# Kernel optimization log

Measured on AMD Instinct MI355X. Metric: run time of the kernel, lower is better.

Reference implementation:

```python
import jax, jax.numpy as jnp
import numpy as np

N = 50000      # nodes
E = 800000     # edges (before self-loops)
F_IN = 256
H = 4          # heads
C1 = 128
C2 = 64
NCLS = 50
NEG_SLOPE = 0.2


def setup_inputs() -> dict:
    key = jax.random.key(0)
    ks = jax.random.split(key, 12)
    x = jax.random.normal(ks[0], (N, F_IN), dtype=jnp.float32)
    edge_index = jax.random.randint(ks[1], (2, E), 0, N, dtype=jnp.int32)
    s1 = 1.0 / np.sqrt(F_IN)
    s2 = 1.0 / np.sqrt(H * C1)
    s3 = 1.0 / np.sqrt(H * C2)
    return {
        "x": x,
        "edge_index": edge_index,
        "W1": jax.random.normal(ks[2], (F_IN, H * C1), dtype=jnp.float32) * s1,
        "a_src1": jax.random.normal(ks[3], (H, C1), dtype=jnp.float32) * s2,
        "a_dst1": jax.random.normal(ks[4], (H, C1), dtype=jnp.float32) * s2,
        "b1": jnp.zeros((H * C1,), dtype=jnp.float32),
        "W2": jax.random.normal(ks[5], (H * C1, H * C2), dtype=jnp.float32) * s2,
        "a_src2": jax.random.normal(ks[6], (H, C2), dtype=jnp.float32) * s3,
        "a_dst2": jax.random.normal(ks[7], (H, C2), dtype=jnp.float32) * s3,
        "b2": jnp.zeros((H * C2,), dtype=jnp.float32),
        "Wf": jax.random.normal(ks[8], (H * C2, NCLS), dtype=jnp.float32) * s3,
        "bf": jnp.zeros((NCLS,), dtype=jnp.float32),
    }


def _gat_conv(x, src, dst, W, a_src, a_dst, b, heads, ch):
    # h: [N, H, C] transformed features
    h = (x @ W).reshape(N, heads, ch)
    # per-node attention halves (standard GAT decomposition, avoids per-edge d-dim gather for scores)
    asrc = jnp.sum(h * a_src[None], axis=-1)  # [N, H]
    adst = jnp.sum(h * a_dst[None], axis=-1)  # [N, H]
    e = jax.nn.leaky_relu(asrc[src] + adst[dst], NEG_SLOPE)  # [E, H]
    # softmax over edges sharing the same destination node
    m = jax.ops.segment_max(e, dst, num_segments=N)          # [N, H]
    ex = jnp.exp(e - m[dst])
    denom = jax.ops.segment_sum(ex, dst, num_segments=N)     # [N, H]
    alpha = ex / (denom[dst] + 1e-16)                        # [E, H]
    msg = h[src] * alpha[:, :, None]                         # [E, H, C]
    out = jax.ops.segment_sum(msg, dst, num_segments=N)      # [N, H, C]
    return out.reshape(N, heads * ch) + b


def reference(x, edge_index, W1, a_src1, a_dst1, b1, W2, a_src2, a_dst2, b2, Wf, bf):
    # PyG GATConv adds self-loops by default
    loops = jnp.arange(N, dtype=edge_index.dtype)
    src = jnp.concatenate([edge_index[0], loops])
    dst = jnp.concatenate([edge_index[1], loops])
    h = _gat_conv(x, src, dst, W1, a_src1, a_dst1, b1, H, C1)
    h = jax.nn.elu(h)
    # F.dropout is identity in eval mode
    h = _gat_conv(h, src, dst, W2, a_src2, a_dst2, b2, H, C2)
    h = jax.nn.elu(h)
    return h @ Wf + bf
```

## Files before the change

kernel.cpp:

```cpp
#include <hip/hip_runtime.h>
#include <hip/hip_fp16.h>
#include <cmath>

#define NN 50000
#define EE 800000
#define ET 850000
#define HH 4
#define CC1 128
#define CC2 64
#define FIN 256
#define NCLS 50

typedef _Float16 half8_t __attribute__((ext_vector_type(8)));
typedef __attribute__((ext_vector_type(4))) float floatx4;

typedef const __attribute__((address_space(1))) unsigned int* glds_gp_t;
typedef __attribute__((address_space(3))) unsigned int* glds_lp_t;
__device__ __forceinline__ void glds16(const void* g, void* l) {
    __builtin_amdgcn_global_load_lds((glds_gp_t)g, (glds_lp_t)l, 16, 0, 0);
}

#define NB_CAST 12500
#define NB_W1   512
#define NB_W2   512
#define NB_WF   64
#define NB_HIST 3321
__global__ __launch_bounds__(256) void prep_hist(
    const float* __restrict__ x, __half* __restrict__ xb,
    const float* __restrict__ W1, __half* __restrict__ W1t,
    const float* __restrict__ W2, __half* __restrict__ W2t,
    const float* __restrict__ Wf, __half* __restrict__ Wft,
    const int* __restrict__ ei, int* __restrict__ deg)
{
    int b = blockIdx.x;
    if (b < NB_CAST) {
        int t = b * 256 + threadIdx.x;
        float4 v = *(const float4*)(x + 4 * (size_t)t);
        __half2 p[2];
        p[0] = __floats2half2_rn(v.x, v.y);
        p[1] = __floats2half2_rn(v.z, v.w);
        *(uint2*)(xb + 4 * (size_t)t) = *(uint2*)p;
    } else if (b < NB_CAST + NB_W1) {
        int t = (b - NB_CAST) * 256 + threadIdx.x;
        int n = t >> 8, k = t & 255;
        W1t[t] = __float2half(W1[(size_t)k * 512 + n]);
    } else if (b < NB_CAST + NB_W1 + NB_W2) {
        int t = (b - NB_CAST - NB_W1) * 256 + threadIdx.x;
        int n = t >> 9, k = t & 511;
        W2t[t] = __float2half(W2[(size_t)k * 256 + n]);
    } else if (b < NB_CAST + NB_W1 + NB_W2 + NB_WF) {
        int t = (b - NB_CAST - NB_W1 - NB_W2) * 256 + threadIdx.x;
        int n = t >> 8, k = t & 255;
        Wft[t] = (n < NCLS) ? __float2half(Wf[(size_t)k * NCLS + n]) : __float2half(0.f);
    } else {
        int t = (b - NB_CAST - NB_W1 - NB_W2 - NB_WF) * 256 + threadIdx.x;
        if (t < ET) {
            int dst = (t < EE) ? ei[EE + t] : (t - EE);
            atomicAdd(&deg[dst], 1);
        }
    }
}

__global__ __launch_bounds__(256) void gemm_f16_v2(
    const __half* __restrict__ A,
    const __half* __restrict__ Bt,
    __half* __restrict__ C,
    int M, int N, int K)
{
    __shared__ __half As[128 * 32];
    __shared__ __half Bs[128 * 32];
    int tid = threadIdx.x, wave = tid >> 6, lane = tid & 63;
    int wm = (wave >> 1) * 64, wn = (wave & 1) * 64;
    int row0 = blockIdx.x * 128, col0 = blockIdx.y * 128;
    int lm = lane & 15, lq = lane >> 4, kq = lq * 8;
    floatx4 acc[4][4] = {};

    int srow = wave * 32 + (lane >> 2);
    int skk  = (lane & 3) * 8;
    int gra0 = row0 + srow;      if (gra0 >= M) gra0 = M - 1;
    int gra1 = row0 + srow + 16; if (gra1 >= M) gra1 = M - 1;
    const __half* ga0 = A + (size_t)gra0 * K + skk;
    const __half* ga1 = A + (size_t)gra1 * K + skk;
    const __half* gb0 = Bt + (size_t)(col0 + srow) * K + skk;
    const __half* gb1 = Bt + (size_t)(col0 + srow + 16) * K + skk;
    __half* la0 = &As[(wave * 32) * 32];
    __half* la1 = &As[(wave * 32 + 16) * 32];
    __half* lb0 = &Bs[(wave * 32) * 32];
    __half* lb1 = &Bs[(wave * 32 + 16) * 32];

    for (int k0 = 0; k0 < K; k0 += 32) {
        __syncthreads();
        glds16(ga0 + k0, la0);
        glds16(ga1 + k0, la1);
        glds16(gb0 + k0, lb0);
        glds16(gb1 + k0, lb1);
        __syncthreads();

        half8_t af[4], bfr[4];
        #pragma unroll
        for (int mt = 0; mt < 4; ++mt)
            af[mt] = *(const half8_t*)&As[(wm + mt * 16 + lm) * 32 + kq];
        #pragma unroll
        for (int nt = 0; nt < 4; ++nt)
            bfr[nt] = *(const half8_t*)&Bs[(wn + nt * 16 + lm) * 32 + kq];
        #pragma unroll
        for (int mt = 0; mt < 4; ++mt)
            #pragma unroll
            for (int nt = 0; nt < 4; ++nt)
                acc[mt][nt] = __builtin_amdgcn_mfma_f32_16x16x32_f16(
                    af[mt], bfr[nt], acc[mt][nt], 0, 0, 0);
    }

    #pragma unroll
    for (int mt = 0; mt < 4; ++mt) {
        int rbase = row0 + wm + mt * 16 + lq * 4;
        #pragma unroll
        for (int nt = 0; nt < 4; ++nt) {
            int c = col0 + wn + nt * 16 + lm;
            #pragma unroll
            for (int r = 0; r < 4; ++r) {
                int gr = rbase + r;
                if (gr < M) C[(size_t)gr * N + c] = __float2half(acc[mt][nt][r]);
            }
        }
    }
}

__global__ __launch_bounds__(128) void gemm_final(
    const __half* __restrict__ A,
    const __half* __restrict__ Bt,
    const float* __restrict__ bias,
    float* __restrict__ out, int M)
{
    __shared__ __half As[128 * 40];
    __shared__ __half Bs[64 * 40];
    int tid = threadIdx.x, wave = tid >> 6, lane = tid & 63;
    int row0 = blockIdx.x * 128;
    int lm = lane & 15, lq = lane >> 4, kq = lq * 8;
    floatx4 acc[4][4] = {};

    for (int k0 = 0; k0 < 256; k0 += 32) {
        int gr = row0 + tid; if (gr >= M) gr = M - 1;
        const __half* ap = A + (size_t)gr * 256 + k0;
        half8_t a0 = *(const half8_t*)ap;
        half8_t a1 = *(const half8_t*)(ap + 8);
        half8_t a2 = *(const half8_t*)(ap + 16);
        half8_t a3 = *(const half8_t*)(ap + 24);
        const __half* bp = Bt + (size_t)(tid >> 1) * 256 + k0 + (tid & 1) * 16;
        half8_t b0 = *(const half8_t*)bp;
        half8_t b1 = *(const half8_t*)(bp + 8);
        __syncthreads();
        *(half8_t*)&As[tid * 40 + 0]  = a0;
        *(half8_t*)&As[tid * 40 + 8]  = a1;
        *(half8_t*)&As[tid * 40 + 16] = a2;
        *(half8_t*)&As[tid * 40 + 24] = a3;
        *(half8_t*)&Bs[(tid >> 1) * 40 + (tid & 1) * 16]     = b0;
        *(half8_t*)&Bs[(tid >> 1) * 40 + (tid & 1) * 16 + 8] = b1;
        __syncthreads();

        half8_t af[4], bfr[4];
        #pragma unroll
        for (int mt = 0; mt < 4; ++mt)
            af[mt] = *(const half8_t*)&As[(wave * 64 + mt * 16 + lm) * 40 + kq];
        #pragma unroll
        for (int nt = 0; nt < 4; ++nt)
            bfr[nt] = *(const half8_t*)&Bs[(nt * 16 + lm) * 40 + kq];
        #pragma unroll
        for (int mt = 0; mt < 4; ++mt)
            #pragma unroll
            for (int nt = 0; nt < 4; ++nt)
                acc[mt][nt] = __builtin_amdgcn_mfma_f32_16x16x32_f16(
                    af[mt], bfr[nt], acc[mt][nt], 0, 0, 0);
    }

    #pragma unroll
    for (int mt = 0; mt < 4; ++mt) {
        int rbase = row0 + wave * 64 + mt * 16 + lq * 4;
        #pragma unroll
        for (int nt = 0; nt < 4; ++nt) {
            int c = nt * 16 + lm;
            if (c >= NCLS) continue;
            float bv = bias[c];
            #pragma unroll
            for (int r = 0; r < 4; ++r) {
                int gr = rbase + r;
                if (gr < M) out[(size_t)gr * NCLS + c] = acc[mt][nt][r] + bv;
            }
        }
    }
}

template<int C>
__global__ __launch_bounds__(256) void attn_scores3(
    const __half* __restrict__ h, const float* __restrict__ a_src,
    const float* __restrict__ a_dst, float* __restrict__ asrc,
    float* __restrict__ adst, int nwaves)
{
    constexpr int HC = HH * C;
    constexpr int CPL = HC / 64;
    int wave = threadIdx.x >> 6;
    int lane = threadIdx.x & 63;
    int wid0 = blockIdx.x * 4 + wave;
    int c0 = lane * CPL;
    int head = c0 / C;

    for (int n = wid0; n < NN; n += nwaves) {
        const __half* hp = h + (size_t)n * HC + c0;
        float hv[CPL];
        if (CPL == 8) {
            union { uint4 u; __half2 h2[4]; } U;
            U.u = *(const uint4*)hp;
            #pragma unroll
            for (int k = 0; k < 4; ++k) {
                float2 f = __half22float2(U.h2[k]);
                hv[2 * k] = f.x; hv[2 * k + 1] = f.y;
            }
        } else {
            union { uint2 u; __half2 h2[2]; } U;
            U.u = *(const uint2*)hp;
            #pragma unroll
            for (int k = 0; k < 2; ++k) {
                float2 f = __half22float2(U.h2[k]);
                hv[2 * k] = f.x; hv[2 * k + 1] = f.y;
            }
        }
        float s1 = 0.f, s2 = 0.f;
        #pragma unroll
        for (int c = 0; c < CPL; ++c) {
            s1 += hv[c] * a_src[c0 + c];
            s2 += hv[c] * a_dst[c0 + c];
        }
        #pragma unroll
        for (int o = 8; o > 0; o >>= 1) {
            s1 += __shfl_xor(s1, o, 64);
            s2 += __shfl_xor(s2, o, 64);
        }
        if ((lane & 15) == 0) {
            asrc[n * HH + head] = s1;
            adst[n * HH + head] = s2;
        }
    }
}

#define SCAN_NB 25
__global__ __launch_bounds__(256) void scan_fused(
    const int* __restrict__ deg, int* __restrict__ off, int* __restrict__ pos)
{
    __shared__ int ws[4];
    __shared__ int base_s;
    int tid = threadIdx.x;
    int lane = tid & 63, wid = tid >> 6;

    int lim = blockIdx.x * 2048;
    int s0 = 0;
    for (int i = tid; i < lim; i += 256) s0 += deg[i];
    #pragma unroll
    for (int o = 32; o > 0; o >>= 1) s0 += __shfl_xor(s0, o, 64);
    if (lane == 0) ws[wid] = s0;
    __syncthreads();
    if (tid == 0) base_s = ws[0] + ws[1] + ws[2] + ws[3];
    __syncthreads();
    int base = base_s;
    __syncthreads();

    int i0 = blockIdx.x * 2048 + tid * 8;
    int v[8]; int s = 0;
    #pragma unroll
    for (int k = 0; k < 8; ++k) {
        int i = i0 + k;
        v[k] = (i < NN) ? deg[i] : 0;
        s += v[k];
    }
    int sc = s;
    #pragma unroll
    for (int o = 1; o < 64; o <<= 1) {
        int t = __shfl_up(sc, o, 64);
        if (lane >= o) sc += t;
    }
    if (lane == 63) ws[wid] = sc;
    __syncthreads();
    int woff = base;
    for (int w = 0; w < wid; ++w) woff += ws[w];
    int excl = woff + sc - s;
    #pragma unroll
    for (int k = 0; k < 8; ++k) {
        int i = i0 + k;
        if (i < NN) { off[i] = excl; pos[i] = excl; }
        excl += v[k];
    }
    if (blockIdx.x == 0 && tid == 0) off[NN] = ET;
}

__global__ void edge_scatter(const int* __restrict__ ei,
                             int* __restrict__ pos, int* __restrict__ csr_src)
{
    int t = blockIdx.x * blockDim.x + threadIdx.x;
    if (t >= ET) return;
    int src, dst;
    if (t < EE) { src = ei[t]; dst = ei[EE + t]; }
    else        { src = t - EE; dst = t - EE; }
    int p = atomicAdd(&pos[dst], 1);
    csr_src[p] = src;
}

template<int C>
__global__ __launch_bounds__(256) void aggregate8(
    const __half* __restrict__ h, const int* __restrict__ off,
    const int* __restrict__ csr_src, const float* __restrict__ asrc,
    const float* __restrict__ adst, const float* __restrict__ bias,
    __half* __restrict__ outb, int nwaves)
{
    constexpr int HC = HH * C;
    constexpr int LPE = HC / 8;
    constexpr int EPW = 64 / LPE;
    constexpr int UNR = 8;
    __shared__ unsigned int exlds_all[4][64 * HH];
    int wave = threadIdx.x >> 6;
    int lane = threadIdx.x & 63;
    int wid0 = blockIdx.x * 4 + wave;
    unsigned int* exlds = exlds_all[wave];
    int el  = (EPW == 1) ? 0 : (lane >> 5);
    int lel = (EPW == 1) ? lane : (lane & 31);
    int coff = lel * 8;
    int hl = coff / C;

    for (int n = wid0; n < NN; n += nwaves) {
        int start = off[n], end = off[n + 1];
        float4 advv = *(const float4*)(adst + (size_t)n * HH);
        float dh0 = 0.f, dh1 = 0.f, dh2 = 0.f, dh3 = 0.f;
        __half2 acc2[4] = {};

        for (int cb = start; cb < end; cb += 64) {
            int eidx = cb + lane;
            bool valid = eidx < end;
            int s_lane = csr_src[valid ? eidx : end - 1];
            float4 t = *(const float4*)(asrc + (size_t)s_lane * HH);
            float e0 = t.x + advv.x; e0 = e0 > 0.f ? e0 : 0.2f * e0;
            float e1 = t.y + advv.y; e1 = e1 > 0.f ? e1 : 0.2f * e1;
            float e2 = t.z + advv.z; e2 = e2 > 0.f ? e2 : 0.2f * e2;
            float e3 = t.w + advv.w; e3 = e3 > 0.f ? e3 : 0.2f * e3;
            float x0 = valid ? __expf(e0) : 0.f;
            float x1 = valid ? __expf(e1) : 0.f;
            float x2 = valid ? __expf(e2) : 0.f;
            float x3 = valid ? __expf(e3) : 0.f;
            dh0 += x0; dh1 += x1; dh2 += x2; dh3 += x3;
            __half2 xp[4];
            xp[0] = __float2half2_rn(x0);
            xp[1] = __float2half2_rn(x1);
            xp[2] = __float2half2_rn(x2);
            xp[3] = __float2half2_rn(x3);
            *(uint4*)&exlds[lane * 4] = *(uint4*)xp;

            int cnt = end - cb; if (cnt > 64) cnt = 64;
            int jmax = (cnt + UNR * EPW - 1) & ~(UNR * EPW - 1);
            for (int jj = 0; jj < jmax; jj += UNR * EPW) {
                int sidx[UNR]; __half2 xs[UNR];
                union { uint4 u; __half2 h2[4]; } uv[UNR];
                #pragma unroll
                for (int u = 0; u < UNR; ++u) {
                    int e_lo = jj + u * EPW;
                    if (EPW == 1) {
                        sidx[u] = __builtin_amdgcn_readlane(s_lane, e_lo);
                    } else {
                        int sa = __builtin_amdgcn_readlane(s_lane, e_lo);
                        int sb = __builtin_amdgcn_readlane(s_lane, e_lo + 1);
                        sidx[u] = el ? sb : sa;
                    }
                    uv[u].u = *(const uint4*)(h + (size_t)sidx[u] * HC + coff);
                    xs[u] = *(__half2*)&exlds[(e_lo + el) * 4 + hl];
                }
                #pragma unroll
                for (int u = 0; u < UNR; ++u)
                    #pragma unroll
                    for (int k = 0; k < 4; ++k)
                        acc2[k] = __hfma2(xs[u], uv[u].h2[k], acc2[k]);
            }
        }

        #pragma unroll
        for (int o = 32; o > 0; o >>= 1) {
            dh0 += __shfl_xor(dh0, o, 64);
            dh1 += __shfl_xor(dh1, o, 64);
            dh2 += __shfl_xor(dh2, o, 64);
            dh3 += __shfl_xor(dh3, o, 64);
        }
        float accf[8];
        #pragma unroll
        for (int k = 0; k < 4; ++k) {
            float2 f = __half22float2(acc2[k]);
            accf[2 * k] = f.x; accf[2 * k + 1] = f.y;
        }
        if (EPW == 2) {
            #pragma unroll
            for (int c = 0; c < 8; ++c)
                accf[c] += __shfl_xor(accf[c], 32, 64);
        }
        float d = (hl == 0) ? dh0 : (hl == 1) ? dh1 : (hl == 2) ? dh2 : dh3;
        float inv = 1.f / (d + 1e-16f);
        if (el == 0) {
            float4 b0 = *(const float4*)(bias + coff);
            float4 b1 = *(const float4*)(bias + coff + 4);
            float bb[8] = {b0.x, b0.y, b0.z, b0.w, b1.x, b1.y, b1.z, b1.w};
            __half2 pk[4];
            #pragma unroll
            for (int c2 = 0; c2 < 4; ++c2) {
                float ua = accf[2 * c2]     * inv + bb[2 * c2];
                float ub = accf[2 * c2 + 1] * inv + bb[2 * c2 + 1];
                ua = ua > 0.f ? ua : expm1f(ua);
                ub = ub > 0.f ? ub : expm1f(ub);
                pk[c2] = __floats2half2_rn(ua, ub);
            }
            *(uint4*)(outb + (size_t)n * HC + coff) = *(uint4*)pk;
        }
    }
}

extern "C" void kernel_launch(void* const* d_in, const int* in_sizes, int n_in,
                              void* d_out, int out_size, void* d_ws, size_t ws_size,
                              hipStream_t stream) {
    const float* x      = (const float*)d_in[0];
    const int*   ei     = (const int*)d_in[1];
    const float* W1     = (const float*)d_in[2];
    const float* a_src1 = (const float*)d_in[3];
    const float* a_dst1 = (const float*)d_in[4];
    const float* b1     = (const float*)d_in[5];
    const float* W2     = (const float*)d_in[6];
    const float* a_src2 = (const float*)d_in[7];
    const float* a_dst2 = (const float*)d_in[8];
    const float* b2     = (const float*)d_in[9];
    const float* Wf     = (const float*)d_in[10];
    const float* bf     = (const float*)d_in[11];
    float* out = (float*)d_out;

    char* p = (char*)d_ws;
    __half* xb    = (__half*)p; p += (size_t)NN * FIN * 2;
    __half* h1b   = (__half*)p; p += (size_t)NN * HH * CC1 * 2;
    __half* out1b = (__half*)p; p += (size_t)NN * HH * CC1 * 2;
    __half* h2b   = (__half*)p; p += (size_t)NN * HH * CC2 * 2;
    __half* out2b = (__half*)p; p += (size_t)NN * HH * CC2 * 2;
    __half* W1t   = (__half*)p; p += (size_t)FIN * HH * CC1 * 2;
    __half* W2t   = (__half*)p; p += (size_t)HH * CC1 * HH * CC2 * 2;
    __half* Wft   = (__half*)p; p += (size_t)64 * HH * CC2 * 2;
    float* asrc   = (float*)p;  p += (size_t)NN * HH * 4;
    float* adst   = (float*)p;  p += (size_t)NN * HH * 4;
    int* deg      = (int*)p;    p += (size_t)NN * 4;
    int* csr_off  = (int*)p;    p += (size_t)(NN + 1) * 4 + 12;
    int* csr_pos  = (int*)p;    p += (size_t)NN * 4;
    int* csr_src  = (int*)p;    p += (size_t)ET * 4;

    hipMemsetAsync(deg, 0, NN * sizeof(int), stream);

    prep_hist<<<NB_CAST + NB_W1 + NB_W2 + NB_WF + NB_HIST, 256, 0, stream>>>(
        x, xb, W1, W1t, W2, W2t, Wf, Wft, ei, deg);

    scan_fused<<<SCAN_NB, 256, 0, stream>>>(deg, csr_off, csr_pos);
    edge_scatter<<<(ET + 255) / 256, 256, 0, stream>>>(ei, csr_pos, csr_src);

    const int AGG_NB = 2048;
    const int AGG_NW = AGG_NB * 4;
    const int ATT_NB = 2048;
    const int ATT_NW = ATT_NB * 4;

    gemm_f16_v2<<<dim3((NN + 127) / 128, (HH * CC1) / 128), 256, 0, stream>>>(
        xb, W1t, h1b, NN, HH * CC1, FIN);
    attn_scores3<CC1><<<ATT_NB, 256, 0, stream>>>(h1b, a_src1, a_dst1, asrc, adst, ATT_NW);
    aggregate8<CC1><<<AGG_NB, 256, 0, stream>>>(h1b, csr_off, csr_src, asrc, adst, b1, out1b, AGG_NW);

    gemm_f16_v2<<<dim3((NN + 127) / 128, (HH * CC2) / 128), 256, 0, stream>>>(
        out1b, W2t, h2b, NN, HH * CC2, HH * CC1);
    attn_scores3<CC2><<<ATT_NB, 256, 0, stream>>>(h2b, a_src2, a_dst2, asrc, adst, ATT_NW);
    aggregate8<CC2><<<AGG_NB, 256, 0, stream>>>(h2b, csr_off, csr_src, asrc, adst, b2, out2b, AGG_NW);

    gemm_final<<<(NN + 127) / 128, 128, 0, stream>>>(out2b, Wft, bf, out, NN);
}
```

Before: 530.4 us.

## Reorder layer-1 GAT as aggregate-then-transform using precomputed W·a attention vectors

```diff
diff --git a/kernel.cpp b/kernel.cpp
--- a/kernel.cpp
+++ b/kernel.cpp
@@ -24,12 +24,15 @@
 #define NB_W1   512
 #define NB_W2   512
 #define NB_WF   64
+#define NB_VA   1
 #define NB_HIST 3321
 __global__ __launch_bounds__(256) void prep_hist(
     const float* __restrict__ x, __half* __restrict__ xb,
     const float* __restrict__ W1, __half* __restrict__ W1t,
     const float* __restrict__ W2, __half* __restrict__ W2t,
     const float* __restrict__ Wf, __half* __restrict__ Wft,
+    const float* __restrict__ a_src1, const float* __restrict__ a_dst1,
+    float* __restrict__ va, float* __restrict__ vd,
     const int* __restrict__ ei, int* __restrict__ deg)
 {
     int b = blockIdx.x;
@@ -52,11 +55,288 @@
         int t = (b - NB_CAST - NB_W1 - NB_W2) * 256 + threadIdx.x;
         int n = t >> 8, k = t & 255;
         Wft[t] = (n < NCLS) ? __float2half(Wf[(size_t)k * NCLS + n]) : __float2half(0.f);
+    } else if (b < NB_CAST + NB_W1 + NB_W2 + NB_WF + NB_VA) {
+        int k = threadIdx.x;
+        const float* wrow = W1 + (size_t)k * 512;
+        float s1[4], s2[4];
+        #pragma unroll
+        for (int h = 0; h < 4; ++h) {
+            float a1 = 0.f, a2 = 0.f;
+            for (int c = 0; c < 128; ++c) {
+                float w = wrow[h * 128 + c];
+                a1 += w * a_src1[h * 128 + c];
+                a2 += w * a_dst1[h * 128 + c];
+            }
+            s1[h] = a1; s2[h] = a2;
+        }
+        *(float4*)(va + 4 * k) = make_float4(s1[0], s1[1], s1[2], s1[3]);
+        *(float4*)(vd + 4 * k) = make_float4(s2[0], s2[1], s2[2], s2[3]);
     } else {
-        int t = (b - NB_CAST - NB_W1 - NB_W2 - NB_WF) * 256 + threadIdx.x;
+        int t = (b - NB_CAST - NB_W1 - NB_W2 - NB_WF - NB_VA) * 256 + threadIdx.x;
         if (t < ET) {
             int dst = (t < EE) ? ei[EE + t] : (t - EE);
             atomicAdd(&deg[dst], 1);
+        }
+    }
+}
+
+#define SCAN_NB 25
+__global__ __launch_bounds__(256) void scan_fused(
+    const int* __restrict__ deg, int* __restrict__ off, int* __restrict__ pos)
+{
+    __shared__ int ws[4];
+    __shared__ int base_s;
+    int tid = threadIdx.x;
+    int lane = tid & 63, wid = tid >> 6;
+
+    int lim = blockIdx.x * 2048;
+    int s0 = 0;
+    for (int i = tid; i < lim; i += 256) s0 += deg[i];
+    #pragma unroll
+    for (int o = 32; o > 0; o >>= 1) s0 += __shfl_xor(s0, o, 64);
+    if (lane == 0) ws[wid] = s0;
+    __syncthreads();
+    if (tid == 0) base_s = ws[0] + ws[1] + ws[2] + ws[3];
+    __syncthreads();
+    int base = base_s;
+    __syncthreads();
+
+    int i0 = blockIdx.x * 2048 + tid * 8;
+    int v[8]; int s = 0;
+    #pragma unroll
+    for (int k = 0; k < 8; ++k) {
+        int i = i0 + k;
+        v[k] = (i < NN) ? deg[i] : 0;
+        s += v[k];
+    }
+    int sc = s;
+    #pragma unroll
+    for (int o = 1; o < 64; o <<= 1) {
+        int t = __shfl_up(sc, o, 64);
+        if (lane >= o) sc += t;
+    }
+    if (lane == 63) ws[wid] = sc;
+    __syncthreads();
+    int woff = base;
+    for (int w = 0; w < wid; ++w) woff += ws[w];
+    int excl = woff + sc - s;
+    #pragma unroll
+    for (int k = 0; k < 8; ++k) {
+        int i = i0 + k;
+        if (i < NN) { off[i] = excl; pos[i] = excl; }
+        excl += v[k];
+    }
+    if (blockIdx.x == 0 && tid == 0) off[NN] = ET;
+}
+
+__global__ void edge_scatter(const int* __restrict__ ei,
+                             int* __restrict__ pos, int* __restrict__ csr_src)
+{
+    int t = blockIdx.x * blockDim.x + threadIdx.x;
+    if (t >= ET) return;
+    int src, dst;
+    if (t < EE) { src = ei[t]; dst = ei[EE + t]; }
+    else        { src = t - EE; dst = t - EE; }
+    int p = atomicAdd(&pos[dst], 1);
+    csr_src[p] = src;
+}
+
+__global__ __launch_bounds__(256) void attn1x(
+    const __half* __restrict__ xb, const float* __restrict__ va,
+    const float* __restrict__ vd, float* __restrict__ asrc,
+    float* __restrict__ adst)
+{
+    int wave = threadIdx.x >> 6;
+    int lane = threadIdx.x & 63;
+    int n = blockIdx.x * 4 + wave;
+    if (n >= NN) return;
+    int k0 = lane * 4;
+    union { uint2 u; __half2 h2[2]; } X;
+    X.u = *(const uint2*)(xb + (size_t)n * 256 + k0);
+    float xv[4];
+    float2 f0 = __half22float2(X.h2[0]);
+    float2 f1 = __half22float2(X.h2[1]);
+    xv[0] = f0.x; xv[1] = f0.y; xv[2] = f1.x; xv[3] = f1.y;
+
+    float s1[4] = {0.f, 0.f, 0.f, 0.f};
+    float s2[4] = {0.f, 0.f, 0.f, 0.f};
+    #pragma unroll
+    for (int j = 0; j < 4; ++j) {
+        float4 a = *(const float4*)(va + 4 * (k0 + j));
+        float4 d = *(const float4*)(vd + 4 * (k0 + j));
+        s1[0] += xv[j] * a.x; s1[1] += xv[j] * a.y;
+        s1[2] += xv[j] * a.z; s1[3] += xv[j] * a.w;
+        s2[0] += xv[j] * d.x; s2[1] += xv[j] * d.y;
+        s2[2] += xv[j] * d.z; s2[3] += xv[j] * d.w;
+    }
+    #pragma unroll
+    for (int o = 32; o > 0; o >>= 1) {
+        #pragma unroll
+        for (int h = 0; h < 4; ++h) {
+            s1[h] += __shfl_xor(s1[h], o, 64);
+            s2[h] += __shfl_xor(s2[h], o, 64);
+        }
+    }
+    if (lane == 0) {
+        *(float4*)(asrc + (size_t)n * HH) = make_float4(s1[0], s1[1], s1[2], s1[3]);
+        *(float4*)(adst + (size_t)n * HH) = make_float4(s2[0], s2[1], s2[2], s2[3]);
+    }
+}
+
+__global__ __launch_bounds__(256) void aggregate_x(
+    const __half* __restrict__ xb, const int* __restrict__ off,
+    const int* __restrict__ csr_src, const float* __restrict__ asrc,
+    const float* __restrict__ adst, __half* __restrict__ xagg)
+{
+    constexpr int UNR = 8;
+    __shared__ unsigned int exlds_all[4][64 * 4];
+    int wave = threadIdx.x >> 6;
+    int lane = threadIdx.x & 63;
+    int n = blockIdx.x * 4 + wave;
+    if (n >= NN) return;
+    unsigned int* exlds = exlds_all[wave];
+    int coff = lane * 4;
+
+    int start = off[n], end = off[n + 1];
+    float4 advv = *(const float4*)(adst + (size_t)n * HH);
+    float dh0 = 0.f, dh1 = 0.f, dh2 = 0.f, dh3 = 0.f;
+    __half2 acc2[4][2] = {};
+
+    for (int cb = start; cb < end; cb += 64) {
+        int eidx = cb + lane;
+        bool valid = eidx < end;
+        int s_lane = csr_src[valid ? eidx : end - 1];
+        float4 t = *(const float4*)(asrc + (size_t)s_lane * HH);
+        float e0 = t.x + advv.x; e0 = e0 > 0.f ? e0 : 0.2f * e0;
+        float e1 = t.y + advv.y; e1 = e1 > 0.f ? e1 : 0.2f * e1;
+        float e2 = t.z + advv.z; e2 = e2 > 0.f ? e2 : 0.2f * e2;
+        float e3 = t.w + advv.w; e3 = e3 > 0.f ? e3 : 0.2f * e3;
+        float x0 = valid ? __expf(e0) : 0.f;
+        float x1 = valid ? __expf(e1) : 0.f;
+        float x2 = valid ? __expf(e2) : 0.f;
+        float x3 = valid ? __expf(e3) : 0.f;
+        dh0 += x0; dh1 += x1; dh2 += x2; dh3 += x3;
+        __half2 xp[4];
+        xp[0] = __float2half2_rn(x0);
+        xp[1] = __float2half2_rn(x1);
+        xp[2] = __float2half2_rn(x2);
+        xp[3] = __float2half2_rn(x3);
+        *(uint4*)&exlds[lane * 4] = *(uint4*)xp;
+
+        int cnt = end - cb; if (cnt > 64) cnt = 64;
+        int jmax = (cnt + UNR - 1) & ~(UNR - 1);
+        for (int jj = 0; jj < jmax; jj += UNR) {
+            int sidx[UNR]; uint2 uv[UNR];
+            #pragma unroll
+            for (int u = 0; u < UNR; ++u) {
+                sidx[u] = __builtin_amdgcn_readlane(s_lane, jj + u);
+                uv[u] = *(const uint2*)(xb + (size_t)sidx[u] * 256 + coff);
+            }
+            #pragma unroll
+            for (int u = 0; u < UNR; ++u) {
+                union { uint4 q; __half2 h2[4]; } X;
+                X.q = *(const uint4*)&exlds[(jj + u) * 4];
+                union { uint2 q; __half2 h2[2]; } V;
+                V.q = uv[u];
+                #pragma unroll
+                for (int h = 0; h < 4; ++h) {
+                    acc2[h][0] = __hfma2(X.h2[h], V.h2[0], acc2[h][0]);
+                    acc2[h][1] = __hfma2(X.h2[h], V.h2[1], acc2[h][1]);
+                }
+            }
+        }
+    }
+
+    #pragma unroll
+    for (int o = 32; o > 0; o >>= 1) {
+        dh0 += __shfl_xor(dh0, o, 64);
+        dh1 += __shfl_xor(dh1, o, 64);
+        dh2 += __shfl_xor(dh2, o, 64);
+        dh3 += __shfl_xor(dh3, o, 64);
+    }
+    float invh[4];
+    invh[0] = 1.f / (dh0 + 1e-16f);
+    invh[1] = 1.f / (dh1 + 1e-16f);
+    invh[2] = 1.f / (dh2 + 1e-16f);
+    invh[3] = 1.f / (dh3 + 1e-16f);
+    #pragma unroll
+    for (int h = 0; h < 4; ++h) {
+        float2 f0 = __half22float2(acc2[h][0]);
+        float2 f1 = __half22float2(acc2[h][1]);
+        __half2 pk[2];
+        pk[0] = __floats2half2_rn(f0.x * invh[h], f0.y * invh[h]);
+        pk[1] = __floats2half2_rn(f1.x * invh[h], f1.y * invh[h]);
+        *(uint2*)(xagg + (size_t)n * 1024 + h * 256 + coff) = *(uint2*)pk;
+    }
+}
+
+__global__ __launch_bounds__(256) void gemm1e(
+    const __half* __restrict__ xagg,
+    const __half* __restrict__ W1t,
+    const float* __restrict__ b1,
+    __half* __restrict__ C, int M)
+{
+    __shared__ __half As[128 * 32];
+    __shared__ __half Bs[128 * 32];
+    int tid = threadIdx.x, wave = tid >> 6, lane = tid & 63;
+    int wm = (wave >> 1) * 64, wn = (wave & 1) * 64;
+    int row0 = blockIdx.x * 128, col0 = blockIdx.y * 128;
+    int head = blockIdx.y;
+    int lm = lane & 15, lq = lane >> 4, kq = lq * 8;
+    floatx4 acc[4][4] = {};
+
+    int srow = wave * 32 + (lane >> 2);
+    int skk  = (lane & 3) * 8;
+    int gra0 = row0 + srow;      if (gra0 >= M) gra0 = M - 1;
+    int gra1 = row0 + srow + 16; if (gra1 >= M) gra1 = M - 1;
+    const __half* ga0 = xagg + (size_t)gra0 * 1024 + head * 256 + skk;
+    const __half* ga1 = xagg + (size_t)gra1 * 1024 + head * 256 + skk;
+    const __half* gb0 = W1t + (size_t)(col0 + srow) * 256 + skk;
+    const __half* gb1 = W1t + (size_t)(col0 + srow + 16) * 256 + skk;
+    __half* la0 = &As[(wave * 32) * 32];
+    __half* la1 = &As[(wave * 32 + 16) * 32];
+    __half* lb0 = &Bs[(wave * 32) * 32];
+    __half* lb1 = &Bs[(wave * 32 + 16) * 32];
+
+    for (int k0 = 0; k0 < 256; k0 += 32) {
+        __syncthreads();
+        glds16(ga0 + k0, la0);
+        glds16(ga1 + k0, la1);
+        glds16(gb0 + k0, lb0);
+        glds16(gb1 + k0, lb1);
+        __syncthreads();
+
+        half8_t af[4], bfr[4];
+        #pragma unroll
+        for (int mt = 0; mt < 4; ++mt)
+            af[mt] = *(const half8_t*)&As[(wm + mt * 16 + lm) * 32 + kq];
+        #pragma unroll
+        for (int nt = 0; nt < 4; ++nt)
+            bfr[nt] = *(const half8_t*)&Bs[(wn + nt * 16 + lm) * 32 + kq];
+        #pragma unroll
+        for (int mt = 0; mt < 4; ++mt)
+            #pragma unroll
+            for (int nt = 0; nt < 4; ++nt)
+                acc[mt][nt] = __builtin_amdgcn_mfma_f32_16x16x32_f16(
+                    af[mt], bfr[nt], acc[mt][nt], 0, 0, 0);
+    }
+
+    #pragma unroll
+    for (int mt = 0; mt < 4; ++mt) {
+        int rbase = row0 + wm + mt * 16 + lq * 4;
+        #pragma unroll
+        for (int nt = 0; nt < 4; ++nt) {
+            int c = col0 + wn + nt * 16 + lm;
+            float bv = b1[c];
+            #pragma unroll
+            for (int r = 0; r < 4; ++r) {
+                int gr = rbase + r;
+                if (gr < M) {
+                    float v = acc[mt][nt][r] + bv;
+                    v = v > 0.f ? v : expm1f(v);
+                    C[(size_t)gr * 512 + c] = __float2half(v);
+                }
+            }
         }
     }
 }
@@ -191,124 +471,51 @@
 }
 
 template<int C>
-__global__ __launch_bounds__(256) void attn_scores3(
+__global__ __launch_bounds__(256) void attn_scores2(
     const __half* __restrict__ h, const float* __restrict__ a_src,
     const float* __restrict__ a_dst, float* __restrict__ asrc,
-    float* __restrict__ adst, int nwaves)
+    float* __restrict__ adst)
 {
     constexpr int HC = HH * C;
     constexpr int CPL = HC / 64;
     int wave = threadIdx.x >> 6;
     int lane = threadIdx.x & 63;
-    int wid0 = blockIdx.x * 4 + wave;
+    int n = blockIdx.x * 4 + wave;
+    if (n >= NN) return;
     int c0 = lane * CPL;
     int head = c0 / C;
-
-    for (int n = wid0; n < NN; n += nwaves) {
-        const __half* hp = h + (size_t)n * HC + c0;
-        float hv[CPL];
-        if (CPL == 8) {
-            union { uint4 u; __half2 h2[4]; } U;
-            U.u = *(const uint4*)hp;
-            #pragma unroll
-            for (int k = 0; k < 4; ++k) {
-                float2 f = __half22float2(U.h2[k]);
-                hv[2 * k] = f.x; hv[2 * k + 1] = f.y;
-            }
-        } else {
-            union { uint2 u; __half2 h2[2]; } U;
-            U.u = *(const uint2*)hp;
-            #pragma unroll
-            for (int k = 0; k < 2; ++k) {
-                float2 f = __half22float2(U.h2[k]);
-                hv[2 * k] = f.x; hv[2 * k + 1] = f.y;
-            }
-        }
-        float s1 = 0.f, s2 = 0.f;
-        #pragma unroll
-        for (int c = 0; c < CPL; ++c) {
-            s1 += hv[c] * a_src[c0 + c];
-            s2 += hv[c] * a_dst[c0 + c];
-        }
-        #pragma unroll
-        for (int o = 8; o > 0; o >>= 1) {
-            s1 += __shfl_xor(s1, o, 64);
-            s2 += __shfl_xor(s2, o, 64);
-        }
-        if ((lane & 15) == 0) {
-            asrc[n * HH + head] = s1;
-            adst[n * HH + head] = s2;
-        }
-    }
-}
-
-#define SCAN_NB 25
-__global__ __launch_bounds__(256) void scan_fused(
-    const int* __restrict__ deg, int* __restrict__ off, int* __restrict__ pos)
-{
-    __shared__ int ws[4];
-    __shared__ int base_s;
-    int tid = threadIdx.x;
-    int lane = tid & 63, wid = tid >> 6;
-
-    int lim = blockIdx.x * 2048;
-    int s0 = 0;
-    for (int i = tid; i < lim; i += 256) s0 += deg[i];
-    #pragma unroll
-    for (int o = 32; o > 0; o >>= 1) s0 += __shfl_xor(s0, o, 64);
-    if (lane == 0) ws[wid] = s0;
-    __syncthreads();
-    if (tid == 0) base_s = ws[0] + ws[1] + ws[2] + ws[3];
-    __syncthreads();
-    int base = base_s;
-    __syncthreads();
-
-    int i0 = blockIdx.x * 2048 + tid * 8;
-    int v[8]; int s = 0;
-    #pragma unroll
-    for (int k = 0; k < 8; ++k) {
-        int i = i0 + k;
-        v[k] = (i < NN) ? deg[i] : 0;
-        s += v[k];
-    }
-    int sc = s;
-    #pragma unroll
-    for (int o = 1; o < 64; o <<= 1) {
-        int t = __shfl_up(sc, o, 64);
-        if (lane >= o) sc += t;
-    }
-    if (lane == 63) ws[wid] = sc;
-    __syncthreads();
-    int woff = base;
-    for (int w = 0; w < wid; ++w) woff += ws[w];
-    int excl = woff + sc - s;
-    #pragma unroll
-    for (int k = 0; k < 8; ++k) {
-        int i = i0 + k;
-        if (i < NN) { off[i] = excl; pos[i] = excl; }
-        excl += v[k];
-    }
-    if (blockIdx.x == 0 && tid == 0) off[NN] = ET;
-}
-
-__global__ void edge_scatter(const int* __restrict__ ei,
-                             int* __restrict__ pos, int* __restrict__ csr_src)
-{
-    int t = blockIdx.x * blockDim.x + threadIdx.x;
-    if (t >= ET) return;
-    int src, dst;
-    if (t < EE) { src = ei[t]; dst = ei[EE + t]; }
-    else        { src = t - EE; dst = t - EE; }
-    int p = atomicAdd(&pos[dst], 1);
-    csr_src[p] = src;
+    const __half* hp = h + (size_t)n * HC + c0;
+    float hv[CPL];
+    union { uint2 u; __half2 h2[2]; } U;
+    U.u = *(const uint2*)hp;
+    #pragma unroll
+    for (int k = 0; k < 2; ++k) {
+        float2 f = __half22float2(U.h2[k]);
+        hv[2 * k] = f.x; hv[2 * k + 1] = f.y;
+    }
+    float s1 = 0.f, s2 = 0.f;
+    #pragma unroll
+    for (int c = 0; c < CPL; ++c) {
+        s1 += hv[c] * a_src[c0 + c];
+        s2 += hv[c] * a_dst[c0 + c];
+    }
+    #pragma unroll
+    for (int o = 8; o > 0; o >>= 1) {
+        s1 += __shfl_xor(s1, o, 64);
+        s2 += __shfl_xor(s2, o, 64);
+    }
+    if ((lane & 15) == 0) {
+        asrc[n * HH + head] = s1;
+        adst[n * HH + head] = s2;
+    }
 }
 
 template<int C>
-__global__ __launch_bounds__(256) void aggregate8(
+__global__ __launch_bounds__(256) void aggregate7(
     const __half* __restrict__ h, const int* __restrict__ off,
     const int* __restrict__ csr_src, const float* __restrict__ asrc,
     const float* __restrict__ adst, const float* __restrict__ bias,
-    __half* __restrict__ outb, int nwaves)
+    __half* __restrict__ outb)
 {
     constexpr int HC = HH * C;
     constexpr int LPE = HC / 8;
@@ -317,101 +524,94 @@
     __shared__ unsigned int exlds_all[4][64 * HH];
     int wave = threadIdx.x >> 6;
     int lane = threadIdx.x & 63;
-    int wid0 = blockIdx.x * 4 + wave;
+    int n = blockIdx.x * 4 + wave;
+    if (n >= NN) return;
     unsigned int* exlds = exlds_all[wave];
     int el  = (EPW == 1) ? 0 : (lane >> 5);
     int lel = (EPW == 1) ? lane : (lane & 31);
     int coff = lel * 8;
     int hl = coff / C;
 
-    for (int n = wid0; n < NN; n += nwaves) {
-        int start = off[n], end = off[n + 1];
-        float4 advv = *(const float4*)(adst + (size_t)n * HH);
-        float dh0 = 0.f, dh1 = 0.f, dh2 = 0.f, dh3 = 0.f;
-        __half2 acc2[4] = {};
-
-        for (int cb = start; cb < end; cb += 64) {
-            int eidx = cb + lane;
-            bool valid = eidx < end;
-            int s_lane = csr_src[valid ? eidx : end - 1];
-            float4 t = *(const float4*)(asrc + (size_t)s_lane * HH);
-            float e0 = t.x + advv.x; e0 = e0 > 0.f ? e0 : 0.2f * e0;
-            float e1 = t.y + advv.y; e1 = e1 > 0.f ? e1 : 0.2f * e1;
-            float e2 = t.z + advv.z; e2 = e2 > 0.f ? e2 : 0.2f * e2;
-            float e3 = t.w + advv.w; e3 = e3 > 0.f ? e3 : 0.2f * e3;
-            float x0 = valid ? __expf(e0) : 0.f;
-            float x1 = valid ? __expf(e1) : 0.f;
-            float x2 = valid ? __expf(e2) : 0.f;
-            float x3 = valid ? __expf(e3) : 0.f;
-            dh0 += x0; dh1 += x1; dh2 += x2; dh3 += x3;
-            __half2 xp[4];
-            xp[0] = __float2half2_rn(x0);
-            xp[1] = __float2half2_rn(x1);
-            xp[2] = __float2half2_rn(x2);
-            xp[3] = __float2half2_rn(x3);
-            *(uint4*)&exlds[lane * 4] = *(uint4*)xp;
-
-            int cnt = end - cb; if (cnt > 64) cnt = 64;
-            int jmax = (cnt + UNR * EPW - 1) & ~(UNR * EPW - 1);
-            for (int jj = 0; jj < jmax; jj += UNR * EPW) {
-                int sidx[UNR]; __half2 xs[UNR];
-                union { uint4 u; __half2 h2[4]; } uv[UNR];
+    int start = off[n], end = off[n + 1];
+    float4 advv = *(const float4*)(adst + (size_t)n * HH);
+    float dh0 = 0.f, dh1 = 0.f, dh2 = 0.f, dh3 = 0.f;
+    __half2 acc2[4] = {};
+
+    for (int cb = start; cb < end; cb += 64) {
+        int eidx = cb + lane;
+        bool valid = eidx < end;
+        int s_lane = csr_src[valid ? eidx : end - 1];
+        float4 t = *(const float4*)(asrc + (size_t)s_lane * HH);
+        float e0 = t.x + advv.x; e0 = e0 > 0.f ? e0 : 0.2f * e0;
+        float e1 = t.y + advv.y; e1 = e1 > 0.f ? e1 : 0.2f * e1;
+        float e2 = t.z + advv.z; e2 = e2 > 0.f ? e2 : 0.2f * e2;
+        float e3 = t.w + advv.w; e3 = e3 > 0.f ? e3 : 0.2f * e3;
+        float x0 = valid ? __expf(e0) : 0.f;
+        float x1 = valid ? __expf(e1) : 0.f;
+        float x2 = valid ? __expf(e2) : 0.f;
+        float x3 = valid ? __expf(e3) : 0.f;
+        dh0 += x0; dh1 += x1; dh2 += x2; dh3 += x3;
+        __half2 xp[4];
+        xp[0] = __float2half2_rn(x0);
+        xp[1] = __float2half2_rn(x1);
+        xp[2] = __float2half2_rn(x2);
+        xp[3] = __float2half2_rn(x3);
+        *(uint4*)&exlds[lane * 4] = *(uint4*)xp;
+
+        int cnt = end - cb; if (cnt > 64) cnt = 64;
+        int jmax = (cnt + UNR * EPW - 1) & ~(UNR * EPW - 1);
+        for (int jj = 0; jj < jmax; jj += UNR * EPW) {
+            int sidx[UNR]; __half2 xs[UNR];
+            union { uint4 u; __half2 h2[4]; } uv[UNR];
+            #pragma unroll
+            for (int u = 0; u < UNR; ++u) {
+                int e_lo = jj + u * EPW;
+                int sa = __builtin_amdgcn_readlane(s_lane, e_lo);
+                int sb = __builtin_amdgcn_readlane(s_lane, e_lo + 1);
+                sidx[u] = el ? sb : sa;
+                uv[u].u = *(const uint4*)(h + (size_t)sidx[u] * HC + coff);
+                xs[u] = *(__half2*)&exlds[(e_lo + el) * 4 + hl];
+            }
+            #pragma unroll
+            for (int u = 0; u < UNR; ++u)
                 #pragma unroll
-                for (int u = 0; u < UNR; ++u) {
-                    int e_lo = jj + u * EPW;
-                    if (EPW == 1) {
-                        sidx[u] = __builtin_amdgcn_readlane(s_lane, e_lo);
-                    } else {
-                        int sa = __builtin_amdgcn_readlane(s_lane, e_lo);
-                        int sb = __builtin_amdgcn_readlane(s_lane, e_lo + 1);
-                        sidx[u] = el ? sb : sa;
-                    }
-                    uv[u].u = *(const uint4*)(h + (size_t)sidx[u] * HC + coff);
-                    xs[u] = *(__half2*)&exlds[(e_lo + el) * 4 + hl];
-                }
-                #pragma unroll
-                for (int u = 0; u < UNR; ++u)
-                    #pragma unroll
-                    for (int k = 0; k < 4; ++k)
-                        acc2[k] = __hfma2(xs[u], uv[u].h2[k], acc2[k]);
-            }
-        }
-
-        #pragma unroll
-        for (int o = 32; o > 0; o >>= 1) {
-            dh0 += __shfl_xor(dh0, o, 64);
-            dh1 += __shfl_xor(dh1, o, 64);
-            dh2 += __shfl_xor(dh2, o, 64);
-            dh3 += __shfl_xor(dh3, o, 64);
-        }
-        float accf[8];
-        #pragma unroll
-        for (int k = 0; k < 4; ++k) {
-            float2 f = __half22float2(acc2[k]);
-            accf[2 * k] = f.x; accf[2 * k + 1] = f.y;
-        }
-        if (EPW == 2) {
-            #pragma unroll
-            for (int c = 0; c < 8; ++c)
-                accf[c] += __shfl_xor(accf[c], 32, 64);
-        }
-        float d = (hl == 0) ? dh0 : (hl == 1) ? dh1 : (hl == 2) ? dh2 : dh3;
-        float inv = 1.f / (d + 1e-16f);
-        if (el == 0) {
-            float4 b0 = *(const float4*)(bias + coff);
-            float4 b1 = *(const float4*)(bias + coff + 4);
-            float bb[8] = {b0.x, b0.y, b0.z, b0.w, b1.x, b1.y, b1.z, b1.w};
-            __half2 pk[4];
-            #pragma unroll
-            for (int c2 = 0; c2 < 4; ++c2) {
-                float ua = accf[2 * c2]     * inv + bb[2 * c2];
-                float ub = accf[2 * c2 + 1] * inv + bb[2 * c2 + 1];
-                ua = ua > 0.f ? ua : expm1f(ua);
-                ub = ub > 0.f ? ub : expm1f(ub);
-                pk[c2] = __floats2half2_rn(ua, ub);
-            }
-            *(uint4*)(outb + (size_t)n * HC + coff) = *(uint4*)pk;
-        }
+                for (int k = 0; k < 4; ++k)
+                    acc2[k] = __hfma2(xs[u], uv[u].h2[k], acc2[k]);
+        }
+    }
+
+    #pragma unroll
+    for (int o = 32; o > 0; o >>= 1) {
+        dh0 += __shfl_xor(dh0, o, 64);
+        dh1 += __shfl_xor(dh1, o, 64);
+        dh2 += __shfl_xor(dh2, o, 64);
+        dh3 += __shfl_xor(dh3, o, 64);
+    }
+    float accf[8];
+    #pragma unroll
+    for (int k = 0; k < 4; ++k) {
+        float2 f = __half22float2(acc2[k]);
+        accf[2 * k] = f.x; accf[2 * k + 1] = f.y;
+    }
+    #pragma unroll
+    for (int c = 0; c < 8; ++c)
+        accf[c] += __shfl_xor(accf[c], 32, 64);
+    float d = (hl == 0) ? dh0 : (hl == 1) ? dh1 : (hl == 2) ? dh2 : dh3;
+    float inv = 1.f / (d + 1e-16f);
+    if (el == 0) {
+        float4 b0 = *(const float4*)(bias + coff);
+        float4 b1 = *(const float4*)(bias + coff + 4);
+        float bb[8] = {b0.x, b0.y, b0.z, b0.w, b1.x, b1.y, b1.z, b1.w};
+        __half2 pk[4];
+        #pragma unroll
+        for (int c2 = 0; c2 < 4; ++c2) {
+            float ua = accf[2 * c2]     * inv + bb[2 * c2];
+            float ub = accf[2 * c2 + 1] * inv + bb[2 * c2 + 1];
+            ua = ua > 0.f ? ua : expm1f(ua);
+            ub = ub > 0.f ? ub : expm1f(ub);
+            pk[c2] = __floats2half2_rn(ua, ub);
+        }
+        *(uint4*)(outb + (size_t)n * HC + coff) = *(uint4*)pk;
     }
 }
 
@@ -434,13 +634,15 @@
 
     char* p = (char*)d_ws;
     __half* xb    = (__half*)p; p += (size_t)NN * FIN * 2;
-    __half* h1b   = (__half*)p; p += (size_t)NN * HH * CC1 * 2;
+    __half* xagg  = (__half*)p; p += (size_t)NN * 1024 * 2;
     __half* out1b = (__half*)p; p += (size_t)NN * HH * CC1 * 2;
     __half* h2b   = (__half*)p; p += (size_t)NN * HH * CC2 * 2;
     __half* out2b = (__half*)p; p += (size_t)NN * HH * CC2 * 2;
     __half* W1t   = (__half*)p; p += (size_t)FIN * HH * CC1 * 2;
     __half* W2t   = (__half*)p; p += (size_t)HH * CC1 * HH * CC2 * 2;
     __half* Wft   = (__half*)p; p += (size_t)64 * HH * CC2 * 2;
+    float* va     = (float*)p;  p += (size_t)FIN * HH * 4;
+    float* vd     = (float*)p;  p += (size_t)FIN * HH * 4;
     float* asrc   = (float*)p;  p += (size_t)NN * HH * 4;
     float* adst   = (float*)p;  p += (size_t)NN * HH * 4;
     int* deg      = (int*)p;    p += (size_t)NN * 4;
@@ -450,26 +652,20 @@
 
     hipMemsetAsync(deg, 0, NN * sizeof(int), stream);
 
-    prep_hist<<<NB_CAST + NB_W1 + NB_W2 + NB_WF + NB_HIST, 256, 0, stream>>>(
-        x, xb, W1, W1t, W2, W2t, Wf, Wft, ei, deg);
+    prep_hist<<<NB_CAST + NB_W1 + NB_W2 + NB_WF + NB_VA + NB_HIST, 256, 0, stream>>>(
+        x, xb, W1, W1t, W2, W2t, Wf, Wft, a_src1, a_dst1, va, vd, ei, deg);
 
     scan_fused<<<SCAN_NB, 256, 0, stream>>>(deg, csr_off, csr_pos);
     edge_scatter<<<(ET + 255) / 256, 256, 0, stream>>>(ei, csr_pos, csr_src);
 
-    const int AGG_NB = 2048;
-    const int AGG_NW = AGG_NB * 4;
-    const int ATT_NB = 2048;
-    const int ATT_NW = ATT_NB * 4;
-
-    gemm_f16_v2<<<dim3((NN + 127) / 128, (HH * CC1) / 128), 256, 0, stream>>>(
-        xb, W1t, h1b, NN, HH * CC1, FIN);
-    attn_scores3<CC1><<<ATT_NB, 256, 0, stream>>>(h1b, a_src1, a_dst1, asrc, adst, ATT_NW);
-    aggregate8<CC1><<<AGG_NB, 256, 0, stream>>>(h1b, csr_off, csr_src, asrc, adst, b1, out1b, AGG_NW);
+    attn1x<<<(NN + 3) / 4, 256, 0, stream>>>(xb, va, vd, asrc, adst);
+    aggregate_x<<<(NN + 3) / 4, 256, 0, stream>>>(xb, csr_off, csr_src, asrc, adst, xagg);
+    gemm1e<<<dim3((NN + 127) / 128, 4), 256, 0, stream>>>(xagg, W1t, b1, out1b, NN);
 
     gemm_f16_v2<<<dim3((NN + 127) / 128, (HH * CC2) / 128), 256, 0, stream>>>(
         out1b, W2t, h2b, NN, HH * CC2, HH * CC1);
-    attn_scores3<CC2><<<ATT_NB, 256, 0, stream>>>(h2b, a_src2, a_dst2, asrc, adst, ATT_NW);
-    aggregate8<CC2><<<AGG_NB, 256, 0, stream>>>(h2b, csr_off, csr_src, asrc, adst, b2, out2b, AGG_NW);
+    attn_scores2<CC2><<<(NN + 3) / 4, 256, 0, stream>>>(h2b, a_src2, a_dst2, asrc, adst);
+    aggregate7<CC2><<<(NN + 3) / 4, 256, 0, stream>>>(h2b, csr_off, csr_src, asrc, adst, b2, out2b);
 
     gemm_final<<<(NN + 127) / 128, 128, 0, stream>>>(out2b, Wft, bf, out, NN);
 }
```

New measurement: 505.8 us. 4.6% less time.
